# Optimization experiments

Hardware: AMD Instinct MI355X
Metric: run time of the kernel (lower is better)

The kernel has to match this reference:

```python
import jax, jax.numpy as jnp
import numpy as np
from jax import lax

B, C, L = 32, 64, 16384
C_OUT = 64


def conv1d(x, w, b):
    # x: [B,C,L], w: [Cout,Cin,K], b: [Cout]
    y = lax.conv_general_dilated(x, w, window_strides=(1,), padding='VALID',
                                 dimension_numbers=('NCH', 'OIH', 'NCH'))
    return y + b[None, :, None]


def setup_inputs() -> dict:
    key = jax.random.key(0)
    k1, k2, k3, k4, k5 = jax.random.split(key, 5)
    x = jax.random.normal(k1, (B, C, L), dtype=jnp.float32)
    # kernel_size = 1 (see shape_source); PyTorch Conv1d default init scale ~ 1/sqrt(Cin*K)
    s = 1.0 / np.sqrt(C * 1)
    offset_w = jax.random.uniform(k2, (C * 1, C, 1), jnp.float32, -s, s)
    offset_b = jax.random.uniform(k3, (C * 1,), jnp.float32, -s, s)
    regular_w = jax.random.uniform(k4, (C_OUT, C, 1), jnp.float32, -s, s)
    regular_b = jax.random.uniform(k5, (C_OUT,), jnp.float32, -s, s)
    return {'x': x, 'offset_w': offset_w, 'offset_b': offset_b,
            'regular_w': regular_w, 'regular_b': regular_b}


def reference(x, offset_w, offset_b, regular_w, regular_b):
    Bx, Cx, Lx = x.shape
    offsets = conv1d(x, offset_w, offset_b)                 # [B,C,L]
    base = jnp.arange(Lx, dtype=x.dtype)[None, None, :]      # [1,1,L]
    indices = jnp.clip(base + offsets, 0.0, Lx - 1)          # [B,C,L] float positions
    idx_floor = jnp.floor(indices)
    idx_ceil = jnp.ceil(indices)
    x_floor = jnp.take_along_axis(x, idx_floor.astype(jnp.int32), axis=2)
    x_ceil = jnp.take_along_axis(x, idx_ceil.astype(jnp.int32), axis=2)
    frac = indices - idx_floor
    x_deform = (1.0 - frac) * x_floor + frac * x_ceil        # [B,C,L]
    return conv1d(x_deform, regular_w, regular_b)            # [B,Cout,L]
```

## Files before the change

kernel.cpp:

```cpp
#include <hip/hip_runtime.h>


#define BDIM 256
#define BB   32
#define CC   64
#define LL   16384
#define TL   64
#define HH   8
#define ROWS (TL + 2*HH)
#define RSW  68
#define RSD  72

#define PERM_HI 0x05040100u
#define PERM_LO 0x07060302u

typedef __attribute__((ext_vector_type(8))) short s8;
typedef __attribute__((ext_vector_type(4))) float f4;

union U32F { unsigned u; float f; };
union S8U  { unsigned u[4]; s8 v; };

static __device__ __forceinline__ unsigned bfround(float f) {
    U32F v; v.f = f;
    return (v.u + 0x7fffu + ((v.u >> 16) & 1u)) >> 16;
}
static __device__ __forceinline__ unsigned packsplit(float f) {
    U32F v; v.f = f;
    unsigned hi = (v.u + 0x7fffu + ((v.u >> 16) & 1u)) >> 16;
    U32F hf; hf.u = hi << 16;
    U32F lv; lv.f = f - hf.f;
    unsigned lo = (lv.u + 0x7fffu + ((lv.u >> 16) & 1u)) >> 16;
    return hi | (lo << 16);
}
static __device__ __forceinline__ float unpackf(unsigned w) {
    U32F a; a.u = w << 16;
    U32F b; b.u = w & 0xffff0000u;
    return a.f + b.f;
}

static __device__ __forceinline__ void load_a_split(const float* __restrict__ wp,
                                                    int row, int ks, int q,
                                                    s8* ahi, s8* alo) {
    const float* base = wp + row * 64 + ks * 32 + q * 8;
    float4 w0 = *(const float4*)base;
    float4 w1 = *(const float4*)(base + 4);
    float vals[8] = {w0.x, w0.y, w0.z, w0.w, w1.x, w1.y, w1.z, w1.w};
    S8U h, l;
    #pragma unroll
    for (int p = 0; p < 4; ++p) {
        unsigned pa = packsplit(vals[2 * p]);
        unsigned pb = packsplit(vals[2 * p + 1]);
        h.u[p] = __builtin_amdgcn_perm(pb, pa, PERM_HI);
        l.u[p] = __builtin_amdgcn_perm(pb, pa, PERM_LO);
    }
    *ahi = h.v; *alo = l.v;
}
static __device__ __forceinline__ s8 load_a_bf16(const float* __restrict__ wp,
                                                 int row, int ks, int q) {
    const float* base = wp + row * 64 + ks * 32 + q * 8;
    float4 w0 = *(const float4*)base;
    float4 w1 = *(const float4*)(base + 4);
    float vals[8] = {w0.x, w0.y, w0.z, w0.w, w1.x, w1.y, w1.z, w1.w};
    S8U r;
    #pragma unroll
    for (int p = 0; p < 4; ++p)
        r.u[p] = bfround(vals[2 * p]) | (bfround(vals[2 * p + 1]) << 16);
    return r.v;
}

__global__ __launch_bounds__(BDIM)
void deform_conv1d_r3(const float* __restrict__ x,
                      const float* __restrict__ offw,
                      const float* __restrict__ offb,
                      const float* __restrict__ regw,
                      const float* __restrict__ regb,
                      float* __restrict__ out) {
    __shared__ __align__(16) unsigned Xt[ROWS * RSW];
    __shared__ __align__(16) unsigned short Xd[TL * RSD];

    const int tid = threadIdx.x;
    const int bx  = blockIdx.x;
    const int lg0 = bx * TL;
    const int b   = blockIdx.y;
    const size_t xb = (size_t)b * CC * LL;

    if (bx >= 1 && bx <= (LL / TL) - 2) {
        for (int i = tid; i < 320; i += BDIM) {
            int cb = i / 20, lb = i - cb * 20;
            int c0 = cb * 4;
            int l0 = lg0 - HH + lb * 4;
            const float* p = x + xb + (size_t)c0 * LL + l0;
            float4 v0 = *(const float4*)(p);
            float4 v1 = *(const float4*)(p + LL);
            float4 v2 = *(const float4*)(p + 2 * LL);
            float4 v3 = *(const float4*)(p + 3 * LL);
            uint4 w;
            w.x = packsplit(v0.x); w.y = packsplit(v1.x);
            w.z = packsplit(v2.x); w.w = packsplit(v3.x);
            *(uint4*)(&Xt[(lb * 4 + 0) * RSW + c0]) = w;
            w.x = packsplit(v0.y); w.y = packsplit(v1.y);
            w.z = packsplit(v2.y); w.w = packsplit(v3.y);
            *(uint4*)(&Xt[(lb * 4 + 1) * RSW + c0]) = w;
            w.x = packsplit(v0.z); w.y = packsplit(v1.z);
            w.z = packsplit(v2.z); w.w = packsplit(v3.z);
            *(uint4*)(&Xt[(lb * 4 + 2) * RSW + c0]) = w;
            w.x = packsplit(v0.w); w.y = packsplit(v1.w);
            w.z = packsplit(v2.w); w.w = packsplit(v3.w);
            *(uint4*)(&Xt[(lb * 4 + 3) * RSW + c0]) = w;
        }
    } else {
        for (int i = tid; i < ROWS * CC; i += BDIM) {
            int r = i >> 6, c = i & 63;
            int g = lg0 - HH + r;
            g = min(max(g, 0), LL - 1);
            Xt[r * RSW + c] = packsplit(x[xb + (size_t)c * LL + g]);
        }
    }
    __syncthreads();

    const int wv   = tid >> 6;
    const int lane = tid & 63;
    const int q    = lane >> 4;
    const int n    = lane & 15;

    s8 ahi[2], alo[2];
    load_a_split(offw, 16 * wv + n, 0, q, &ahi[0], &alo[0]);
    load_a_split(offw, 16 * wv + n, 1, q, &ahi[1], &alo[1]);

    f4 acc[4];
    {
        float4 bo = *(const float4*)(offb + 16 * wv + 4 * q);
        #pragma unroll
        for (int nt = 0; nt < 4; ++nt) acc[nt] = (f4){bo.x, bo.y, bo.z, bo.w};
    }
    #pragma unroll
    for (int nt = 0; nt < 4; ++nt) {
        const int row = HH + 16 * nt + n;
        #pragma unroll
        for (int ks = 0; ks < 2; ++ks) {
            const unsigned* bp = &Xt[row * RSW + ks * 32 + q * 8];
            uint4 wlo = *(const uint4*)(bp);
            uint4 whi = *(const uint4*)(bp + 4);
            unsigned wd[8] = {wlo.x, wlo.y, wlo.z, wlo.w,
                              whi.x, whi.y, whi.z, whi.w};
            S8U bh, bl;
            #pragma unroll
            for (int p = 0; p < 4; ++p) {
                bh.u[p] = __builtin_amdgcn_perm(wd[2 * p + 1], wd[2 * p], PERM_HI);
                bl.u[p] = __builtin_amdgcn_perm(wd[2 * p + 1], wd[2 * p], PERM_LO);
            }
            acc[nt] = __builtin_amdgcn_mfma_f32_16x16x32_bf16(ahi[ks], bh.v, acc[nt], 0, 0, 0);
            acc[nt] = __builtin_amdgcn_mfma_f32_16x16x32_bf16(ahi[ks], bl.v, acc[nt], 0, 0, 0);
            acc[nt] = __builtin_amdgcn_mfma_f32_16x16x32_bf16(alo[ks], bh.v, acc[nt], 0, 0, 0);
        }
    }

    #pragma unroll
    for (int nt = 0; nt < 4; ++nt) {
        #pragma unroll
        for (int reg = 0; reg < 4; ++reg) {
            const int c = 16 * wv + 4 * q + reg;
            const int l = lg0 + 16 * nt + n;
            float o  = acc[nt][reg];
            float of = floorf(o);
            float fr = o - of;
            int idx  = l + (int)of;
            if (idx < 0)            { idx = 0;      fr = 0.0f; }
            else if (idx >= LL - 1) { idx = LL - 1; fr = 0.0f; }
            int u = idx - lg0 + HH;
            float x0, x1;
            if ((unsigned)u <= (unsigned)(ROWS - 2)) {
                x0 = unpackf(Xt[u * RSW + c]);
                x1 = unpackf(Xt[(u + 1) * RSW + c]);
            } else {
                const float* xr = x + xb + (size_t)c * LL;
                x0 = xr[idx];
                x1 = xr[idx + (fr > 0.0f ? 1 : 0)];
            }
            acc[nt][reg] = x0 + fr * (x1 - x0);
        }
    }

    #pragma unroll
    for (int nt = 0; nt < 4; ++nt) {
        unsigned h0 = bfround(acc[nt][0]);
        unsigned h1 = bfround(acc[nt][1]);
        unsigned h2 = bfround(acc[nt][2]);
        unsigned h3 = bfround(acc[nt][3]);
        uint2 pw;
        pw.x = h0 | (h1 << 16);
        pw.y = h2 | (h3 << 16);
        *(uint2*)(&Xd[(16 * nt + n) * RSD + 16 * wv + 4 * q]) = pw;
    }
    __syncthreads();

    s8 a2[2];
    a2[0] = load_a_bf16(regw, 16 * wv + n, 0, q);
    a2[1] = load_a_bf16(regw, 16 * wv + n, 1, q);
    {
        float4 br = *(const float4*)(regb + 16 * wv + 4 * q);
        #pragma unroll
        for (int nt = 0; nt < 4; ++nt) acc[nt] = (f4){br.x, br.y, br.z, br.w};
    }
    #pragma unroll
    for (int nt = 0; nt < 4; ++nt) {
        #pragma unroll
        for (int ks = 0; ks < 2; ++ks) {
            s8 bv = *(const s8*)(&Xd[(16 * nt + n) * RSD + ks * 32 + q * 8]);
            acc[nt] = __builtin_amdgcn_mfma_f32_16x16x32_bf16(a2[ks], bv, acc[nt], 0, 0, 0);
        }
    }

    float* op = out + (size_t)b * CC * LL;
    #pragma unroll
    for (int nt = 0; nt < 4; ++nt) {
        #pragma unroll
        for (int reg = 0; reg < 4; ++reg) {
            op[(size_t)(16 * wv + 4 * q + reg) * LL + lg0 + 16 * nt + n] = acc[nt][reg];
        }
    }
}

extern "C" void kernel_launch(void* const* d_in, const int* in_sizes, int n_in,
                              void* d_out, int out_size, void* d_ws, size_t ws_size,
                              hipStream_t stream) {
    const float* x    = (const float*)d_in[0];
    const float* offw = (const float*)d_in[1];
    const float* offb = (const float*)d_in[2];
    const float* regw = (const float*)d_in[3];
    const float* regb = (const float*)d_in[4];
    float* out = (float*)d_out;

    dim3 grid(LL / TL, BB);
    deform_conv1d_r3<<<grid, dim3(BDIM), 0, stream>>>(x, offw, offb, regw, regb, out);
}
```

Baseline: 260.7 us.

## Switch to fp16 split MFMA with pre-split swizzled LDS tiles and fp16 gather buffer

Replaces bf16 hi/lo packed words with separate fp16 hi and lo tiles stored in XOR-swizzled LDS layouts, so the MFMA B operands load directly without per-element perm repacking. The gather source moves to a separate channel-major fp16 buffer, and the deformed tile reuses the first LDS region. The clamp logic is simplified with fmed3, and the weight loads are moved before the barrier. The gather now reads fp16-rounded x instead of the split hi+lo value, which lowers interpolation precision, and the fp16 range limits could affect accuracy.

```diff
diff --git a/kernel.cpp b/kernel.cpp
--- a/kernel.cpp
+++ b/kernel.cpp
@@ -8,75 +8,62 @@
 #define TL   64
 #define HH   8
 #define ROWS (TL + 2*HH)
-#define RSW  68
-#define RSD  72
-
-#define PERM_HI 0x05040100u
-#define PERM_LO 0x07060302u
-
-typedef __attribute__((ext_vector_type(8))) short s8;
+#define RSW  36
+#define XGS  82
+
+typedef __fp16 half_t;
+typedef __attribute__((ext_vector_type(2))) __fp16 h2;
+typedef __attribute__((ext_vector_type(8))) __fp16 h8;
 typedef __attribute__((ext_vector_type(4))) float f4;
 
-union U32F { unsigned u; float f; };
-union S8U  { unsigned u[4]; s8 v; };
-
-static __device__ __forceinline__ unsigned bfround(float f) {
-    U32F v; v.f = f;
-    return (v.u + 0x7fffu + ((v.u >> 16) & 1u)) >> 16;
-}
-static __device__ __forceinline__ unsigned packsplit(float f) {
-    U32F v; v.f = f;
-    unsigned hi = (v.u + 0x7fffu + ((v.u >> 16) & 1u)) >> 16;
-    U32F hf; hf.u = hi << 16;
-    U32F lv; lv.f = f - hf.f;
-    unsigned lo = (lv.u + 0x7fffu + ((lv.u >> 16) & 1u)) >> 16;
-    return hi | (lo << 16);
-}
-static __device__ __forceinline__ float unpackf(unsigned w) {
-    U32F a; a.u = w << 16;
-    U32F b; b.u = w & 0xffff0000u;
-    return a.f + b.f;
+union H2U { h2 h; unsigned u; };
+union H8U { unsigned u[4]; h8 v; };
+
+static __device__ __forceinline__ unsigned pk(float a, float b) {
+    H2U r; r.h = __builtin_amdgcn_cvt_pkrtz(a, b); return r.u;
 }
 
 static __device__ __forceinline__ void load_a_split(const float* __restrict__ wp,
                                                     int row, int ks, int q,
-                                                    s8* ahi, s8* alo) {
+                                                    h8* ahi, h8* alo) {
     const float* base = wp + row * 64 + ks * 32 + q * 8;
     float4 w0 = *(const float4*)base;
     float4 w1 = *(const float4*)(base + 4);
-    float vals[8] = {w0.x, w0.y, w0.z, w0.w, w1.x, w1.y, w1.z, w1.w};
-    S8U h, l;
+    float v[8] = {w0.x, w0.y, w0.z, w0.w, w1.x, w1.y, w1.z, w1.w};
+    H8U h, l;
     #pragma unroll
     for (int p = 0; p < 4; ++p) {
-        unsigned pa = packsplit(vals[2 * p]);
-        unsigned pb = packsplit(vals[2 * p + 1]);
-        h.u[p] = __builtin_amdgcn_perm(pb, pa, PERM_HI);
-        l.u[p] = __builtin_amdgcn_perm(pb, pa, PERM_LO);
+        H2U hh; hh.h = __builtin_amdgcn_cvt_pkrtz(v[2*p], v[2*p+1]);
+        h.u[p] = hh.u;
+        l.u[p] = pk(v[2*p] - (float)hh.h[0], v[2*p+1] - (float)hh.h[1]);
     }
     *ahi = h.v; *alo = l.v;
 }
-static __device__ __forceinline__ s8 load_a_bf16(const float* __restrict__ wp,
-                                                 int row, int ks, int q) {
+
+static __device__ __forceinline__ h8 load_a_f16(const float* __restrict__ wp,
+                                                int row, int ks, int q) {
     const float* base = wp + row * 64 + ks * 32 + q * 8;
     float4 w0 = *(const float4*)base;
     float4 w1 = *(const float4*)(base + 4);
-    float vals[8] = {w0.x, w0.y, w0.z, w0.w, w1.x, w1.y, w1.z, w1.w};
-    S8U r;
-    #pragma unroll
-    for (int p = 0; p < 4; ++p)
-        r.u[p] = bfround(vals[2 * p]) | (bfround(vals[2 * p + 1]) << 16);
+    float v[8] = {w0.x, w0.y, w0.z, w0.w, w1.x, w1.y, w1.z, w1.w};
+    H8U r;
+    #pragma unroll
+    for (int p = 0; p < 4; ++p) r.u[p] = pk(v[2*p], v[2*p+1]);
     return r.v;
 }
 
 __global__ __launch_bounds__(BDIM)
-void deform_conv1d_r3(const float* __restrict__ x,
+void deform_conv1d_r4(const float* __restrict__ x,
                       const float* __restrict__ offw,
                       const float* __restrict__ offb,
                       const float* __restrict__ regw,
                       const float* __restrict__ regb,
                       float* __restrict__ out) {
-    __shared__ __align__(16) unsigned Xt[ROWS * RSW];
-    __shared__ __align__(16) unsigned short Xd[TL * RSD];
+    __shared__ __align__(16) unsigned char smem[9216 + 9216 + 10496];
+    unsigned* XtH = (unsigned*)smem;
+    unsigned* XtL = (unsigned*)(smem + 9216);
+    half_t*   Xg  = (half_t*)(smem + 18432);
+    unsigned* XdW = (unsigned*)smem;
 
     const int tid = threadIdx.x;
     const int bx  = blockIdx.x;
@@ -89,89 +76,110 @@
             int cb = i / 20, lb = i - cb * 20;
             int c0 = cb * 4;
             int l0 = lg0 - HH + lb * 4;
-            const float* p = x + xb + (size_t)c0 * LL + l0;
-            float4 v0 = *(const float4*)(p);
-            float4 v1 = *(const float4*)(p + LL);
-            float4 v2 = *(const float4*)(p + 2 * LL);
-            float4 v3 = *(const float4*)(p + 3 * LL);
-            uint4 w;
-            w.x = packsplit(v0.x); w.y = packsplit(v1.x);
-            w.z = packsplit(v2.x); w.w = packsplit(v3.x);
-            *(uint4*)(&Xt[(lb * 4 + 0) * RSW + c0]) = w;
-            w.x = packsplit(v0.y); w.y = packsplit(v1.y);
-            w.z = packsplit(v2.y); w.w = packsplit(v3.y);
-            *(uint4*)(&Xt[(lb * 4 + 1) * RSW + c0]) = w;
-            w.x = packsplit(v0.z); w.y = packsplit(v1.z);
-            w.z = packsplit(v2.z); w.w = packsplit(v3.z);
-            *(uint4*)(&Xt[(lb * 4 + 2) * RSW + c0]) = w;
-            w.x = packsplit(v0.w); w.y = packsplit(v1.w);
-            w.z = packsplit(v2.w); w.w = packsplit(v3.w);
-            *(uint4*)(&Xt[(lb * 4 + 3) * RSW + c0]) = w;
+            const float* pp = x + xb + (size_t)c0 * LL + l0;
+            float4 v0 = *(const float4*)(pp);
+            float4 v1 = *(const float4*)(pp + LL);
+            float4 v2 = *(const float4*)(pp + 2 * LL);
+            float4 v3 = *(const float4*)(pp + 3 * LL);
+            unsigned* gw = (unsigned*)Xg;
+            int wi = 41 * c0 + 2 * lb;
+            gw[wi]       = pk(v0.x, v0.y); gw[wi + 1]   = pk(v0.z, v0.w);
+            gw[wi + 41]  = pk(v1.x, v1.y); gw[wi + 42]  = pk(v1.z, v1.w);
+            gw[wi + 82]  = pk(v2.x, v2.y); gw[wi + 83]  = pk(v2.z, v2.w);
+            gw[wi + 123] = pk(v3.x, v3.y); gw[wi + 124] = pk(v3.z, v3.w);
+            if (lb >= 2 && lb < 18) {
+                int m = lb - 2;
+                float e0[4] = {v0.x, v0.y, v0.z, v0.w};
+                float e1[4] = {v1.x, v1.y, v1.z, v1.w};
+                float e2[4] = {v2.x, v2.y, v2.z, v2.w};
+                float e3[4] = {v3.x, v3.y, v3.z, v3.w};
+                int blkw  = (cb >> 1) ^ (m & 7);
+                int wbase = (4 * m) * RSW + (blkw << 2) + 2 * (cb & 1);
+                #pragma unroll
+                for (int rl = 0; rl < 4; ++rl) {
+                    float a = e0[rl], bb = e1[rl], cc = e2[rl], dd = e3[rl];
+                    H2U h0, h1;
+                    h0.h = __builtin_amdgcn_cvt_pkrtz(a, bb);
+                    h1.h = __builtin_amdgcn_cvt_pkrtz(cc, dd);
+                    int widx = wbase + rl * RSW;
+                    uint2 hw; hw.x = h0.u; hw.y = h1.u;
+                    *(uint2*)&XtH[widx] = hw;
+                    uint2 lw;
+                    lw.x = pk(a  - (float)h0.h[0], bb - (float)h0.h[1]);
+                    lw.y = pk(cc - (float)h1.h[0], dd - (float)h1.h[1]);
+                    *(uint2*)&XtL[widx] = lw;
+                }
+            }
         }
     } else {
         for (int i = tid; i < ROWS * CC; i += BDIM) {
             int r = i >> 6, c = i & 63;
-            int g = lg0 - HH + r;
-            g = min(max(g, 0), LL - 1);
-            Xt[r * RSW + c] = packsplit(x[xb + (size_t)c * LL + g]);
-        }
-    }
-    __syncthreads();
+            int g = min(max(lg0 - HH + r, 0), LL - 1);
+            float v = x[xb + (size_t)c * LL + g];
+            H2U hv; hv.h = __builtin_amdgcn_cvt_pkrtz(v, 0.0f);
+            Xg[c * XGS + r] = hv.h[0];
+            int row = r - HH;
+            if (row >= 0 && row < TL) {
+                int blkw = (c >> 3) ^ ((row >> 2) & 7);
+                int widx = row * RSW + (blkw << 2) + ((c >> 1) & 3);
+                float lo = v - (float)hv.h[0];
+                H2U lv; lv.h = __builtin_amdgcn_cvt_pkrtz(lo, 0.0f);
+                ((half_t*)XtH)[2 * widx + (c & 1)] = hv.h[0];
+                ((half_t*)XtL)[2 * widx + (c & 1)] = lv.h[0];
+            }
+        }
+    }
 
     const int wv   = tid >> 6;
     const int lane = tid & 63;
     const int q    = lane >> 4;
     const int n    = lane & 15;
 
-    s8 ahi[2], alo[2];
+    h8 ahi[2], alo[2];
     load_a_split(offw, 16 * wv + n, 0, q, &ahi[0], &alo[0]);
     load_a_split(offw, 16 * wv + n, 1, q, &ahi[1], &alo[1]);
-
     f4 acc[4];
     {
         float4 bo = *(const float4*)(offb + 16 * wv + 4 * q);
         #pragma unroll
         for (int nt = 0; nt < 4; ++nt) acc[nt] = (f4){bo.x, bo.y, bo.z, bo.w};
     }
-    #pragma unroll
-    for (int nt = 0; nt < 4; ++nt) {
-        const int row = HH + 16 * nt + n;
+    __syncthreads();
+
+    #pragma unroll
+    for (int nt = 0; nt < 4; ++nt) {
+        const int row = 16 * nt + n;
+        const int rb  = row * RSW;
+        const int sb  = (row >> 2) & 7;
         #pragma unroll
         for (int ks = 0; ks < 2; ++ks) {
-            const unsigned* bp = &Xt[row * RSW + ks * 32 + q * 8];
-            uint4 wlo = *(const uint4*)(bp);
-            uint4 whi = *(const uint4*)(bp + 4);
-            unsigned wd[8] = {wlo.x, wlo.y, wlo.z, wlo.w,
-                              whi.x, whi.y, whi.z, whi.w};
-            S8U bh, bl;
-            #pragma unroll
-            for (int p = 0; p < 4; ++p) {
-                bh.u[p] = __builtin_amdgcn_perm(wd[2 * p + 1], wd[2 * p], PERM_HI);
-                bl.u[p] = __builtin_amdgcn_perm(wd[2 * p + 1], wd[2 * p], PERM_LO);
-            }
-            acc[nt] = __builtin_amdgcn_mfma_f32_16x16x32_bf16(ahi[ks], bh.v, acc[nt], 0, 0, 0);
-            acc[nt] = __builtin_amdgcn_mfma_f32_16x16x32_bf16(ahi[ks], bl.v, acc[nt], 0, 0, 0);
-            acc[nt] = __builtin_amdgcn_mfma_f32_16x16x32_bf16(alo[ks], bh.v, acc[nt], 0, 0, 0);
-        }
-    }
-
-    #pragma unroll
-    for (int nt = 0; nt < 4; ++nt) {
+            int blk = (4 * ks + q) ^ sb;
+            h8 bh = *(const h8*)&XtH[rb + (blk << 2)];
+            h8 bl = *(const h8*)&XtL[rb + (blk << 2)];
+            acc[nt] = __builtin_amdgcn_mfma_f32_16x16x32_f16(ahi[ks], bh, acc[nt], 0, 0, 0);
+            acc[nt] = __builtin_amdgcn_mfma_f32_16x16x32_f16(ahi[ks], bl, acc[nt], 0, 0, 0);
+            acc[nt] = __builtin_amdgcn_mfma_f32_16x16x32_f16(alo[ks], bh, acc[nt], 0, 0, 0);
+        }
+    }
+
+    #pragma unroll
+    for (int nt = 0; nt < 4; ++nt) {
+        const int l = lg0 + 16 * nt + n;
         #pragma unroll
         for (int reg = 0; reg < 4; ++reg) {
             const int c = 16 * wv + 4 * q + reg;
-            const int l = lg0 + 16 * nt + n;
             float o  = acc[nt][reg];
-            float of = floorf(o);
-            float fr = o - of;
-            int idx  = l + (int)of;
-            if (idx < 0)            { idx = 0;      fr = 0.0f; }
-            else if (idx >= LL - 1) { idx = LL - 1; fr = 0.0f; }
-            int u = idx - lg0 + HH;
+            float p  = (float)l + o;
+            p = __builtin_amdgcn_fmed3f(p, 0.0f, (float)(LL - 1));
+            float of = floorf(p);
+            float fr = p - of;
+            int idx  = (int)of;
+            int u    = idx - lg0 + HH;
             float x0, x1;
             if ((unsigned)u <= (unsigned)(ROWS - 2)) {
-                x0 = unpackf(Xt[u * RSW + c]);
-                x1 = unpackf(Xt[(u + 1) * RSW + c]);
+                const half_t* gp = Xg + c * XGS + u;
+                x0 = (float)gp[0];
+                x1 = (float)gp[1];
             } else {
                 const float* xr = x + xb + (size_t)c * LL;
                 x0 = xr[idx];
@@ -181,33 +189,38 @@
         }
     }
 
-    #pragma unroll
-    for (int nt = 0; nt < 4; ++nt) {
-        unsigned h0 = bfround(acc[nt][0]);
-        unsigned h1 = bfround(acc[nt][1]);
-        unsigned h2 = bfround(acc[nt][2]);
-        unsigned h3 = bfround(acc[nt][3]);
+    __syncthreads();
+
+    #pragma unroll
+    for (int nt = 0; nt < 4; ++nt) {
+        const int row = 16 * nt + n;
+        const int sb  = (row >> 2) & 7;
+        const int bw  = (2 * wv + (q >> 1)) ^ sb;
         uint2 pw;
-        pw.x = h0 | (h1 << 16);
-        pw.y = h2 | (h3 << 16);
-        *(uint2*)(&Xd[(16 * nt + n) * RSD + 16 * wv + 4 * q]) = pw;
-    }
-    __syncthreads();
-
-    s8 a2[2];
-    a2[0] = load_a_bf16(regw, 16 * wv + n, 0, q);
-    a2[1] = load_a_bf16(regw, 16 * wv + n, 1, q);
+        pw.x = pk(acc[nt][0], acc[nt][1]);
+        pw.y = pk(acc[nt][2], acc[nt][3]);
+        *(uint2*)&XdW[row * RSW + (bw << 2) + 2 * (q & 1)] = pw;
+    }
+
+    h8 a2[2];
+    a2[0] = load_a_f16(regw, 16 * wv + n, 0, q);
+    a2[1] = load_a_f16(regw, 16 * wv + n, 1, q);
     {
         float4 br = *(const float4*)(regb + 16 * wv + 4 * q);
         #pragma unroll
         for (int nt = 0; nt < 4; ++nt) acc[nt] = (f4){br.x, br.y, br.z, br.w};
     }
-    #pragma unroll
-    for (int nt = 0; nt < 4; ++nt) {
+    __syncthreads();
+
+    #pragma unroll
+    for (int nt = 0; nt < 4; ++nt) {
+        const int row = 16 * nt + n;
+        const int sb  = (row >> 2) & 7;
         #pragma unroll
         for (int ks = 0; ks < 2; ++ks) {
-            s8 bv = *(const s8*)(&Xd[(16 * nt + n) * RSD + ks * 32 + q * 8]);
-            acc[nt] = __builtin_amdgcn_mfma_f32_16x16x32_bf16(a2[ks], bv, acc[nt], 0, 0, 0);
+            int blk = (4 * ks + q) ^ sb;
+            h8 bv = *(const h8*)&XdW[row * RSW + (blk << 2)];
+            acc[nt] = __builtin_amdgcn_mfma_f32_16x16x32_f16(a2[ks], bv, acc[nt], 0, 0, 0);
         }
     }
 
@@ -232,5 +245,5 @@
     float* out = (float*)d_out;
 
     dim3 grid(LL / TL, BB);
-    deform_conv1d_r3<<<grid, dim3(BDIM), 0, stream>>>(x, offw, offb, regw, regb, out);
-}
+    deform_conv1d_r4<<<grid, dim3(BDIM), 0, stream>>>(x, offw, offb, regw, regb, out);
+}
```

Result: slower. 271.6 us (+4.2%).
